# Optimization experiments

Measured on AMD Instinct MI355X. Metric: run time of the kernel, lower is better.

The kernel has to match this reference:

```python
import jax, jax.numpy as jnp
import numpy as np

PRE_NMS_TOPK = 6000
POST_NMS_TOPK = 1000
NMS_THRESH = 0.7
MIN_SIZE = 16.0
NEG = -1e9  # stand-in for -inf that is safe under autodiff


def setup_inputs() -> dict:
    key = jax.random.key(0)
    k1, k2, k3, k4, k5, k6, k7, k8 = jax.random.split(key, 8)
    B, A = 8, 200000
    N = B * A
    # realistic anchors: centers within a ~1333x800 canvas, sizes 16..256
    cx = jax.random.uniform(k1, (N,), minval=0.0, maxval=1200.0)
    cy = jax.random.uniform(k2, (N,), minval=0.0, maxval=800.0)
    w = jax.random.uniform(k3, (N,), minval=16.0, maxval=256.0)
    h = jax.random.uniform(k4, (N,), minval=16.0, maxval=256.0)
    anchors = jnp.stack([cx - 0.5 * w, cy - 0.5 * h, cx + 0.5 * w, cy + 0.5 * h], axis=1)
    batch_indices = jnp.sort(jax.random.randint(k5, (N,), 0, B)).astype(jnp.int32)
    image_sizes = jax.random.randint(k6, (B, 2), 600, 1334).astype(jnp.int32)  # (H, W)
    objectness_logits = jax.random.normal(k7, (N, 1), dtype=jnp.float32)
    bbox_deltas = jax.random.normal(k8, (N, 4), dtype=jnp.float32) * 0.2
    return {
        'anchors': anchors,
        'batch_indices': batch_indices,
        'image_sizes': image_sizes,
        'objectness_logits': objectness_logits,
        'bbox_deltas': bbox_deltas,
    }


def _nms_one(bx, sc):
    """Greedy NMS on [K,4] boxes / [K] scores; returns POST_NMS_TOPK (idx, ok)."""
    K = bx.shape[0]
    areas = (bx[:, 2] - bx[:, 0]) * (bx[:, 3] - bx[:, 1])
    ar = jnp.arange(K)

    def step(sup, _):
        s = jnp.where(sup, NEG, sc)
        j = jnp.argmax(s)
        ok = s[j] > 0.5 * NEG
        b = bx[j]
        ix1 = jnp.maximum(b[0], bx[:, 0])
        iy1 = jnp.maximum(b[1], bx[:, 1])
        ix2 = jnp.minimum(b[2], bx[:, 2])
        iy2 = jnp.minimum(b[3], bx[:, 3])
        inter = jnp.maximum(ix2 - ix1, 0.0) * jnp.maximum(iy2 - iy1, 0.0)
        iou = inter / (areas + areas[j] - inter + 1e-9)
        sup = sup | (iou > NMS_THRESH) | (ar == j)
        return sup, (j, ok)

    sup0 = sc <= 0.5 * NEG  # padded / invalid entries start suppressed
    _, (idx, ok) = jax.lax.scan(step, sup0, None, length=POST_NMS_TOPK)
    return idx, ok


def reference(anchors, batch_indices, image_sizes, objectness_logits, bbox_deltas):
    B = image_sizes.shape[0]
    N = anchors.shape[0]
    sizes = image_sizes[batch_indices].astype(jnp.float32)  # [N,2] (H,W) per anchor

    # --- box decode ---
    a_w = anchors[:, 2] - anchors[:, 0]
    a_h = anchors[:, 3] - anchors[:, 1]
    a_x = anchors[:, 0] + 0.5 * a_w
    a_y = anchors[:, 1] + 0.5 * a_h
    t_x, t_y = bbox_deltas[:, 0], bbox_deltas[:, 1]
    t_w, t_h = bbox_deltas[:, 2], bbox_deltas[:, 3]
    p_x = a_x + t_x * a_w
    p_y = a_y + t_y * a_h
    p_w = a_w * jnp.exp(jnp.clip(t_w, -10.0, 10.0))
    p_h = a_h * jnp.exp(jnp.clip(t_h, -10.0, 10.0))
    x1 = p_x - 0.5 * p_w
    y1 = p_y - 0.5 * p_h
    x2 = p_x + 0.5 * p_w
    y2 = p_y + 0.5 * p_h

    # --- clip to image ---
    H, W = sizes[:, 0], sizes[:, 1]
    x1 = jnp.clip(x1, 0.0, W - 1.0)
    y1 = jnp.clip(y1, 0.0, H - 1.0)
    x2 = jnp.clip(x2, 0.0, W - 1.0)
    y2 = jnp.clip(y2, 0.0, H - 1.0)
    boxes = jnp.stack([x1, y1, x2, y2], axis=1)  # [N,4]

    # --- min-size filter (as score masking) ---
    valid = ((x2 - x1) >= MIN_SIZE) & ((y2 - y1) >= MIN_SIZE)
    fg = jax.nn.sigmoid(objectness_logits[:, 0])

    # --- per-image top-k over masked scores ---
    img_mask = batch_indices[None, :] == jnp.arange(B, dtype=batch_indices.dtype)[:, None]  # [B,N]
    scores = jnp.where(img_mask & valid[None, :], fg[None, :], NEG)  # [B,N]
    top_scores, top_idx = jax.lax.top_k(scores, PRE_NMS_TOPK)  # [B,PRE]
    top_boxes = boxes[top_idx]  # [B,PRE,4]

    # --- NMS per image ---
    keep_idx, keep_ok = jax.vmap(_nms_one)(top_boxes, top_scores)  # [B,POST]

    sel = jnp.take_along_axis(top_idx, keep_idx, axis=1)  # global anchor indices [B,POST]
    okf = keep_ok[..., None].astype(boxes.dtype)
    props = jnp.take_along_axis(top_boxes, keep_idx[..., None], axis=1) * okf  # [B,POST,4]
    obj = objectness_logits[sel] * okf  # [B,POST,1]
    deltas_out = bbox_deltas[sel] * okf  # [B,POST,4]
    bidx = jnp.where(keep_ok, jnp.arange(B, dtype=jnp.int32)[:, None], -1)  # [B,POST]

    return (props.reshape(-1, 4), bidx.reshape(-1), obj.reshape(-1, 1),
            deltas_out.reshape(-1, 4), keep_ok.reshape(-1))
```

## Files before the change

### kernel.cpp

```cpp
#include <hip/hip_runtime.h>
#include <stdint.h>

#define PRE_K   6000
#define POST_K  1000
#define CAP     8192
#define BINS    1024
#define ROWS    6016
#define CH      94
#define RC_CH   32
#define JSPLIT  8
#define NEGF    -1000000000.0f
#define IOU_EPS 16.0f


__device__ __forceinline__ uint32_t orderf(float f) {
  uint32_t u = __float_as_uint(f);
  return (u & 0x80000000u) ? ~u : (u | 0x80000000u);
}

__device__ __forceinline__ int score_bin(float sc) {
  int bin = (int)floorf((sc + 12.0f) * ((float)BINS / 24.0f));
  return bin < 0 ? 0 : (bin > BINS - 1 ? BINS - 1 : bin);
}

__device__ __forceinline__ int bin_slot(int bin) {
  return ((bin & 15) << 6) | (bin >> 4);
}

__device__ __forceinline__ void decode_box(
    const float* __restrict__ anchors, const float* __restrict__ deltas,
    const int* __restrict__ isz, int n, int b,
    double& x1, double& y1, double& x2, double& y2, bool& valid) {
  double ax1 = (double)anchors[4 * n + 0], ay1 = (double)anchors[4 * n + 1];
  double ax2 = (double)anchors[4 * n + 2], ay2 = (double)anchors[4 * n + 3];
  double aw = ax2 - ax1, ah = ay2 - ay1;
  double acx = ax1 + 0.5 * aw, acy = ay1 + 0.5 * ah;
  double tx = (double)deltas[4 * n + 0], ty = (double)deltas[4 * n + 1];
  double tw = (double)deltas[4 * n + 2], th = (double)deltas[4 * n + 3];
  tw = tw < -10.0 ? -10.0 : (tw > 10.0 ? 10.0 : tw);
  th = th < -10.0 ? -10.0 : (th > 10.0 ? 10.0 : th);
  double px = acx + tx * aw, py = acy + ty * ah;
  double pw = aw * exp(tw), ph = ah * exp(th);
  double H = (double)isz[2 * b + 0], W = (double)isz[2 * b + 1];
  double wm = W - 1.0, hm = H - 1.0;
  x1 = px - 0.5 * pw; y1 = py - 0.5 * ph;
  x2 = px + 0.5 * pw; y2 = py + 0.5 * ph;
  x1 = fmin(fmax(x1, 0.0), wm); x2 = fmin(fmax(x2, 0.0), wm);
  y1 = fmin(fmax(y1, 0.0), hm); y2 = fmin(fmax(y2, 0.0), hm);
  valid = (x2 - x1 >= 16.0) && (y2 - y1 >= 16.0);
}

__device__ __forceinline__ bool iou_exact(const double* __restrict__ tbox,
                                          const double* __restrict__ tarea,
                                          size_t ri, size_t ci) {
  const double* pr = &tbox[ri * 4];
  const double* pc = &tbox[ci * 4];
  double w = fmin(pr[2], pc[2]) - fmax(pr[0], pc[0]); w = w > 0.0 ? w : 0.0;
  double h = fmin(pr[3], pc[3]) - fmax(pr[1], pc[1]); h = h > 0.0 ? h : 0.0;
  double it = w * h;
  return it > 0.7 * (tarea[ri] + tarea[ci] - it + 1e-9);
}


__global__ void __launch_bounds__(256) k_score(const float* __restrict__ anchors,
                                               const int* __restrict__ bix,
                                               const int* __restrict__ isz,
                                               const float* __restrict__ logits,
                                               const float* __restrict__ deltas,
                                               float* __restrict__ scores,
                                               uint32_t* __restrict__ hist, int N) {
  const int SPAN = 4096;
  int start = blockIdx.x * SPAN;
  int end = start + SPAN < N ? start + SPAN : N;
  __shared__ uint32_t lh[2][BINS];
  for (int i = threadIdx.x; i < 2 * BINS; i += 256) ((uint32_t*)lh)[i] = 0u;
  __shared__ int s_b0, s_b1;
  if (threadIdx.x == 0) { s_b0 = bix[start]; s_b1 = bix[end - 1]; }
  __syncthreads();
  int b0 = s_b0, b1 = s_b1;

  for (int n = start + (int)threadIdx.x; n < end; n += 256) {
    int b = bix[n];
    double x1, y1, x2, y2; bool valid;
    decode_box(anchors, deltas, isz, n, b, x1, y1, x2, y2, valid);
    float sc = valid ? logits[n] : NEGF;
    scores[n] = sc;
    if (valid) {
      int bin = score_bin(sc);
      if (b == b0)      atomicAdd(&lh[0][bin], 1u);
      else if (b == b1) atomicAdd(&lh[1][bin], 1u);
      else              atomicAdd(&hist[b * BINS + bin_slot(bin)], 1u);
    }
  }
  __syncthreads();
  for (int bin = threadIdx.x; bin < BINS; bin += 256) {
    uint32_t c0 = lh[0][bin];
    if (c0) atomicAdd(&hist[b0 * BINS + bin_slot(bin)], c0);
    if (b1 != b0) {
      uint32_t c1 = lh[1][bin];
      if (c1) atomicAdd(&hist[b1 * BINS + bin_slot(bin)], c1);
    }
  }
}

__global__ void __launch_bounds__(1024) k_compact(const float* __restrict__ scores,
                                                  const int* __restrict__ bix,
                                                  const uint32_t* __restrict__ hist,
                                                  uint32_t* __restrict__ cnt,
                                                  uint64_t* __restrict__ cand, int N) {
  const int SPAN = 8192;
  int start = blockIdx.x * SPAN;
  int end = start + SPAN < N ? start + SPAN : N;
  int t = threadIdx.x;
  __shared__ int s_b0, s_b1;
  __shared__ uint32_t sh[BINS];
  __shared__ int s_bs;
  __shared__ uint32_t lcnt[8], lbase[8];
  if (t == 0) { s_b0 = bix[start]; s_b1 = bix[end - 1]; }
  if (t < 8) lcnt[t] = 0u;
  __syncthreads();
  int b0 = s_b0, b1 = s_b1;

  uint32_t bs0 = 0, bs1 = 0;
  for (int pass = 0; pass < 2; pass++) {
    int b = pass == 0 ? b0 : b1;
    if (pass == 1 && b1 == b0) { bs1 = bs0; break; }
    if (t < BINS) sh[t] = hist[b * BINS + bin_slot(t)];
    if (t == 0) s_bs = 0;
    __syncthreads();
    for (int off = 1; off < BINS; off <<= 1) {
      uint32_t v = (t < BINS && t + off < BINS) ? sh[t + off] : 0u;
      __syncthreads();
      if (t < BINS) sh[t] += v;
      __syncthreads();
    }
    if (t < BINS && sh[t] >= PRE_K) atomicMax(&s_bs, t);
    __syncthreads();
    if (pass == 0) bs0 = (uint32_t)s_bs; else bs1 = (uint32_t)s_bs;
    __syncthreads();
  }

  bool     predv[8];
  uint64_t keyv[8];
  uint32_t lposv[8];
  int      bv[8];
  int nt = 0;
  for (int base = start; base < end; base += 1024, nt++) {
    int n = base + t;
    bool pred = false; int b = 0; uint64_t key = 0ull; uint32_t lp = 0u;
    if (n < end) {
      float sc = scores[n];
      if (sc > 0.5f * NEGF) {
        b = bix[n];
        uint32_t bs = (b == b0) ? bs0 : bs1;
        if ((uint32_t)score_bin(sc) >= bs) {
          pred = true;
          key = ((uint64_t)orderf(sc) << 32) | (uint64_t)(uint32_t)(~(uint32_t)n);
          lp = atomicAdd(&lcnt[b], 1u);
        }
      }
    }
    predv[nt] = pred; keyv[nt] = key; lposv[nt] = lp; bv[nt] = b;
  }
  __syncthreads();
  if (t < 8) {
    uint32_t c = lcnt[t];
    lbase[t] = c ? atomicAdd(&cnt[t], c) : 0u;
  }
  __syncthreads();
  for (int k = 0; k < nt; k++) {
    if (predv[k]) {
      uint32_t pos = lbase[bv[k]] + lposv[k];
      if (pos < CAP) cand[(size_t)bv[k] * CAP + pos] = keyv[k];
    }
  }
}

__global__ void __launch_bounds__(256) k_rank(const uint64_t* __restrict__ cand,
                                              const uint32_t* __restrict__ cnt,
                                              uint32_t* __restrict__ prank) {
  int blk = blockIdx.x;
  int js = blk % JSPLIT;
  int ic = (blk / JSPLIT) % 32;
  int b  = blk / (JSPLIT * 32);
  int t = threadIdx.x;
  int C = (int)min(cnt[b], (uint32_t)CAP);
  if (ic * 256 >= C) return;
  const uint64_t* g = cand + (size_t)b * CAP;
  int i = ic * 256 + t;
  uint64_t ki = (i < C) ? g[i] : 0ull;

  int q = (C + JSPLIT - 1) / JSPLIT;
  int j0 = js * q;
  int j1 = j0 + q < C ? j0 + q : C;

  __shared__ uint64_t tile[1024];
  int rank = 0;
  for (int base = j0; base < j1; base += 1024) {
#pragma unroll
    for (int u = 0; u < 4; u++) {
      int j = base + u * 256 + t;
      tile[u * 256 + t] = (j < j1) ? g[j] : 0ull;
    }
    __syncthreads();
    int lim = j1 - base < 1024 ? j1 - base : 1024;
    const ulonglong2* t2 = (const ulonglong2*)tile;
    int pairs = lim >> 1;
    int jj = 0;
    for (; jj + 4 <= pairs; jj += 4) {
      ulonglong2 v0 = t2[jj + 0], v1 = t2[jj + 1];
      ulonglong2 v2 = t2[jj + 2], v3 = t2[jj + 3];
      rank += (v0.x > ki) ? 1 : 0; rank += (v0.y > ki) ? 1 : 0;
      rank += (v1.x > ki) ? 1 : 0; rank += (v1.y > ki) ? 1 : 0;
      rank += (v2.x > ki) ? 1 : 0; rank += (v2.y > ki) ? 1 : 0;
      rank += (v3.x > ki) ? 1 : 0; rank += (v3.y > ki) ? 1 : 0;
    }
    for (; jj < pairs; jj++) {
      ulonglong2 v = t2[jj];
      rank += (v.x > ki) ? 1 : 0; rank += (v.y > ki) ? 1 : 0;
    }
    if (lim & 1) rank += (tile[lim - 1] > ki) ? 1 : 0;
    __syncthreads();
  }
  if (i < C) prank[((size_t)b * JSPLIT + js) * CAP + i] = (uint32_t)rank;
}

__global__ void __launch_bounds__(256) k_place_gather(
    const uint64_t* __restrict__ cand, const uint32_t* __restrict__ cnt,
    const uint32_t* __restrict__ prank,
    const float* __restrict__ anchors, const float* __restrict__ deltas,
    const int* __restrict__ isz,
    double* __restrict__ tbox, double* __restrict__ tarea,
    float4* __restrict__ tboxf, float* __restrict__ tareaf,
    int* __restrict__ top_n, int* __restrict__ Cnum, int B) {
  int idx = blockIdx.x * blockDim.x + threadIdx.x;
  if (idx >= B * CAP) return;
  int b = idx / CAP, i = idx % CAP;
  int C = (int)min(cnt[b], (uint32_t)CAP);
  if (i == 0) Cnum[b] = C < PRE_K ? C : PRE_K;
  if (i >= C) return;
  uint32_t rank = 0;
#pragma unroll
  for (int js = 0; js < JSPLIT; js++)
    rank += prank[((size_t)b * JSPLIT + js) * CAP + i];
  if (rank >= PRE_K) return;
  int n = (int)(~(uint32_t)(cand[idx] & 0xFFFFFFFFull));
  double x1, y1, x2, y2; bool valid;
  decode_box(anchors, deltas, isz, n, b, x1, y1, x2, y2, valid);
  size_t row = (size_t)b * ROWS + rank;
  tbox[row * 4 + 0] = x1;
  tbox[row * 4 + 1] = y1;
  tbox[row * 4 + 2] = x2;
  tbox[row * 4 + 3] = y2;
  double ar = (x2 - x1) * (y2 - y1);
  tarea[row] = ar;
  tboxf[row] = make_float4((float)x1, (float)y1, (float)x2, (float)y2);
  tareaf[row] = (float)ar;
  top_n[b * PRE_K + rank] = n;
}

__global__ void __launch_bounds__(64) k_iou_mat(const float4* __restrict__ tboxf,
                                                const float* __restrict__ tareaf,
                                                const double* __restrict__ tbox,
                                                const double* __restrict__ tarea,
                                                const int* __restrict__ Cnum,
                                                uint32_t* __restrict__ maskT) {
  int blk = blockIdx.x;
  int k  = blk % (RC_CH + 1);
  int cc = (blk / (RC_CH + 1)) % CH;
  int b  = blk / ((RC_CH + 1) * CH);
  int rc = (k == RC_CH) ? cc : k;
  if (k < RC_CH && cc <= rc) return;
  int C = Cnum[b];
  if (rc * 64 >= C || cc * 64 >= C) return;
  int lane = threadIdx.x;
  size_t bb = (size_t)b * ROWS;

  float4 cb4 = tboxf[bb + (size_t)cc * 64 + lane];
  float  sca = 0.7f * tareaf[bb + (size_t)cc * 64 + lane];
  __shared__ float4 rbx[64];
  __shared__ float  rsa[64];
  rbx[lane] = tboxf[bb + (size_t)rc * 64 + lane];
  rsa[lane] = 0.7f * tareaf[bb + (size_t)rc * 64 + lane];
  __syncthreads();

  bool isdiag = (rc == cc);
  uint32_t res0 = 0u, res1 = 0u;

  for (int i = 0; i < 64; i++) {
    float4 r4 = rbx[i];
    float sra = rsa[i];
    float iw = fminf(r4.z, cb4.z) - fmaxf(r4.x, cb4.x);
    float ih = fminf(r4.w, cb4.w) - fmaxf(r4.y, cb4.y);
    iw = fmaxf(iw, 0.0f); ih = fmaxf(ih, 0.0f);
    float inter = iw * ih;
    float diff = fmaf(1.7f, inter, -(sra + sca));
    bool gt = isdiag ? (lane > i) : true;
    unsigned long long sup   = __ballot(gt && (diff >  IOU_EPS));
    unsigned long long loose = __ballot(gt && (diff > -IOU_EPS));
    unsigned long long border = loose & ~sup;
    if (border) {
      bool mine = (border >> lane) & 1ull;
      bool ex = false;
      if (mine)
        ex = iou_exact(tbox, tarea, bb + (size_t)rc * 64 + i,
                       bb + (size_t)cc * 64 + lane);
      sup |= __ballot(ex);
    }
    if (lane == i) { res0 = (uint32_t)sup; res1 = (uint32_t)(sup >> 32); }
  }
  uint2* seg = (uint2*)(maskT + (((size_t)b * CH + cc) * ROWS + (size_t)rc * 64) * 2);
  seg[lane] = make_uint2(res0, res1);
}

__global__ void __launch_bounds__(256) k_nms_reduce(const uint32_t* __restrict__ maskT,
                                                    const float4* __restrict__ tboxf,
                                                    const float* __restrict__ tareaf,
                                                    const double* __restrict__ tbox,
                                                    const double* __restrict__ tarea,
                                                    const int* __restrict__ Cnum,
                                                    const int* __restrict__ top_n,
                                                    const float* __restrict__ logits,
                                                    const float* __restrict__ deltas,
                                                    float* __restrict__ out, int B) {
  int b = blockIdx.x, t = threadIdx.x;
  int wave = t >> 6, lane = t & 63;
  int C = Cnum[b];
  const uint32_t* M = maskT + (size_t)b * CH * ROWS * 2;
  size_t bb = (size_t)b * ROWS;

  __shared__ uint32_t s_f[2][2];
  __shared__ uint32_t kept_lo[POST_K];
  __shared__ uint32_t kept_hi[POST_K];
  __shared__ uint64_t s_kept;
  if (t < 4) ((uint32_t*)s_f)[t] = 0u;

  uint32_t d0 = 0u, d1 = 0u;
  if (wave == 0) {
    const uint32_t* rp = M + (size_t)lane * 2;
    d0 = rp[0]; d1 = rp[1];
  }
  __syncthreads();

  int nkept = 0, nlo = 0, nhi = 0;
  for (int c = 0; c < CH; c++) {
    int base = c * 64;
    if (base >= C) break;
    int cbuf = c & 1;
    if (t == 0) { s_f[cbuf ^ 1][0] = 0u; s_f[cbuf ^ 1][1] = 0u; }

    uint32_t f0 = 0u, f1 = 0u;
    for (int k2 = t; k2 < nlo; k2 += 256) {
      const uint32_t* rp = M + ((size_t)c * ROWS + kept_lo[k2]) * 2;
      f0 |= rp[0]; f1 |= rp[1];
    }
    if (nhi > 0) {
      float4 cb4 = tboxf[bb + base + lane];
      float  sca = 0.7f * tareaf[bb + base + lane];
      for (int k2 = wave; k2 < nhi; k2 += 4) {
        int r = (int)kept_hi[k2];
        float4 r4 = tboxf[bb + r];
        float sra = 0.7f * tareaf[bb + r];
        float iw = fminf(r4.z, cb4.z) - fmaxf(r4.x, cb4.x);
        float ih = fminf(r4.w, cb4.w) - fmaxf(r4.y, cb4.y);
        iw = fmaxf(iw, 0.0f); ih = fmaxf(ih, 0.0f);
        float inter = iw * ih;
        float diff = fmaf(1.7f, inter, -(sra + sca));
        unsigned long long sup   = __ballot(diff >  IOU_EPS);
        unsigned long long loose = __ballot(diff > -IOU_EPS);
        unsigned long long border = loose & ~sup;
        if (border) {
          bool mine = (border >> lane) & 1ull;
          bool ex = false;
          if (mine) ex = iou_exact(tbox, tarea, bb + r, bb + base + lane);
          sup |= __ballot(ex);
        }
        f0 |= (uint32_t)sup; f1 |= (uint32_t)(sup >> 32);
      }
    }
#pragma unroll
    for (int off = 32; off > 0; off >>= 1) {
      f0 |= (uint32_t)__shfl_xor((int)f0, off, 64);
      f1 |= (uint32_t)__shfl_xor((int)f1, off, 64);
    }
    if (lane == 0 && (f0 | f1)) {
      atomicOr(&s_f[cbuf][0], f0);
      atomicOr(&s_f[cbuf][1], f1);
    }
    __syncthreads();

    if (wave == 0) {
      uint64_t sup = (uint64_t)s_f[cbuf][0] | ((uint64_t)s_f[cbuf][1] << 32);
      int rem = C - base;
      if (rem < 64) sup |= ~((1ull << rem) - 1ull);
      uint64_t diag = (uint64_t)d0 | ((uint64_t)d1 << 32);
      int cn = (c + 1 < CH) ? c + 1 : c;
      const uint32_t* rpn = M + ((size_t)cn * ROWS + (size_t)cn * 64 + lane) * 2;
      uint32_t pn0 = rpn[0], pn1 = rpn[1];

      uint64_t keptMask = 0ull;
      uint64_t alive = ~sup;
      uint64_t m = alive;
      while (m) {
        int i = __builtin_ctzll(m);
        keptMask |= 1ull << i;
        uint64_t d = (uint64_t)__shfl((long long)diag, i, 64);
        sup |= d | (1ull << i);
        m = alive & ~sup;
      }
      int allowed = POST_K - nkept;
      int pc = __popcll(keptMask);
      while (pc > allowed) {
        keptMask &= ~(1ull << (63 - __builtin_clzll(keptMask)));
        pc--;
      }
      if (lane == 0) s_kept = keptMask;
      if ((keptMask >> lane) & 1ull) {
        int pfx = __popcll(keptMask & ((1ull << lane) - 1ull));
        int row = base + lane;
        if (c < RC_CH) kept_lo[nlo + pfx] = (uint32_t)row;
        else           kept_hi[nhi + pfx] = (uint32_t)row;
      }
      d0 = pn0; d1 = pn1;
    }
    __syncthreads();

    int pc = __popcll(s_kept);
    nkept += pc;
    if (c < RC_CH) nlo += pc; else nhi += pc;
    if (nkept >= POST_K) break;
  }

  __syncthreads();
  int M_out = B * POST_K;
  for (int s2 = t; s2 < POST_K; s2 += 256) {
    float p0 = 0.f, p1 = 0.f, p2 = 0.f, p3 = 0.f;
    float ob = 0.f, d0f = 0.f, d1f = 0.f, d2f = 0.f, d3f = 0.f;
    float bi = -1.0f, okv = 0.0f;
    if (s2 < nkept) {
      int j = (s2 < nlo) ? (int)kept_lo[s2] : (int)kept_hi[s2 - nlo];
      int n = top_n[b * PRE_K + j];
      const double* p = &tbox[(bb + j) * 4];
      p0 = (float)p[0]; p1 = (float)p[1]; p2 = (float)p[2]; p3 = (float)p[3];
      ob = logits[n];
      d0f = deltas[4 * n + 0]; d1f = deltas[4 * n + 1];
      d2f = deltas[4 * n + 2]; d3f = deltas[4 * n + 3];
      bi = (float)b; okv = 1.0f;
    }
    int idx = b * POST_K + s2;
    out[idx * 4 + 0] = p0;
    out[idx * 4 + 1] = p1;
    out[idx * 4 + 2] = p2;
    out[idx * 4 + 3] = p3;
    out[4 * M_out + idx] = bi;
    out[5 * M_out + idx] = ob;
    out[6 * M_out + idx * 4 + 0] = d0f;
    out[6 * M_out + idx * 4 + 1] = d1f;
    out[6 * M_out + idx * 4 + 2] = d2f;
    out[6 * M_out + idx * 4 + 3] = d3f;
    out[10 * M_out + idx] = okv;
  }
}


extern "C" void kernel_launch(void* const* d_in, const int* in_sizes, int n_in,
                              void* d_out, int out_size, void* d_ws, size_t ws_size,
                              hipStream_t stream) {
  const float* anchors = (const float*)d_in[0];
  const int*   bix     = (const int*)d_in[1];
  const int*   isz     = (const int*)d_in[2];
  const float* logits  = (const float*)d_in[3];
  const float* deltas  = (const float*)d_in[4];
  float* out = (float*)d_out;

  int N = in_sizes[1];
  int B = in_sizes[2] / 2;

  uintptr_t p = (uintptr_t)d_ws;
  double*   tbox   = (double*)p;    p += (size_t)B * ROWS * 4 * sizeof(double);
  double*   tarea  = (double*)p;    p += (size_t)B * ROWS * sizeof(double);
  uint64_t* cand   = (uint64_t*)p;  p += (size_t)B * CAP * sizeof(uint64_t);
  float*    scores = (float*)p;     p += (size_t)N * sizeof(float);
  uint32_t* hist   = (uint32_t*)p;  p += (size_t)B * BINS * sizeof(uint32_t);
  uint32_t* cnt    = (uint32_t*)p;  p += (size_t)B * sizeof(uint32_t);
  uint32_t* prank  = (uint32_t*)p;  p += (size_t)B * JSPLIT * CAP * sizeof(uint32_t);
  int*      top_n    = (int*)p;     p += (size_t)B * PRE_K * sizeof(int);
  int*      Cnum     = (int*)p;      p += (size_t)B * sizeof(int);
  p = (p + 255) & ~(uintptr_t)255;
  uint32_t* maskT    = (uint32_t*)p; p += (size_t)B * CH * ROWS * 2 * sizeof(uint32_t);
  float4*   tboxf  = (float4*)scores;
  float*    tareaf = (float*)(scores + (size_t)B * ROWS * 4);
  (void)ws_size; (void)n_in; (void)out_size;

  hipMemsetAsync(hist, 0, (size_t)(B * BINS + B) * sizeof(uint32_t), stream);
  k_score<<<(N + 4095) / 4096, 256, 0, stream>>>(anchors, bix, isz, logits, deltas,
                                                 scores, hist, N);
  k_compact<<<(N + 8191) / 8192, 1024, 0, stream>>>(scores, bix, hist, cnt, cand, N);
  k_rank<<<B * 32 * JSPLIT, 256, 0, stream>>>(cand, cnt, prank);
  k_place_gather<<<(B * CAP + 255) / 256, 256, 0, stream>>>(cand, cnt, prank,
                                                            anchors, deltas, isz,
                                                            tbox, tarea, tboxf,
                                                            tareaf, top_n, Cnum, B);
  k_iou_mat<<<B * CH * (RC_CH + 1), 64, 0, stream>>>(tboxf, tareaf, tbox, tarea,
                                                     Cnum, maskT);
  k_nms_reduce<<<B, 256, 0, stream>>>(maskT, tboxf, tareaf, tbox, tarea, Cnum,
                                      top_n, logits, deltas, out, B);
}
```

Before: 353.5 us.

## Compute full upper-triangular IoU mask and push suppression forward during NMS scan

The IoU mask kernel now fills every upper-triangular 64x64 tile over a 3D grid, replacing the hybrid where only the first 32 row chunks were precomputed and later chunks recomputed IoU on the fly. The NMS reduce kernel changes from pulling kept rows per chunk to pushing them forward. Rows kept in chunk c are OR-ed into per-chunk shared accumulators for all later chunks by waves 1-3, while wave 0 resolves chunk c+1 using the next-chunk rows it prefetched. This removes the on-the-fly IoU recomputation and overlaps mask accumulation with the serial greedy scan. In exchange it computes a much larger mask (about 94*95/2 tiles per image), which costs more memory traffic and more shared-memory atomics.

```diff
diff --git a/kernel.cpp b/kernel.cpp
--- a/kernel.cpp
+++ b/kernel.cpp
@@ -7,7 +7,6 @@
 #define BINS    1024
 #define ROWS    6016
 #define CH      94
-#define RC_CH   32
 #define JSPLIT  8
 #define NEGF    -1000000000.0f
 #define IOU_EPS 16.0f
@@ -265,14 +264,12 @@
                                                 const double* __restrict__ tarea,
                                                 const int* __restrict__ Cnum,
                                                 uint32_t* __restrict__ maskT) {
-  int blk = blockIdx.x;
-  int k  = blk % (RC_CH + 1);
-  int cc = (blk / (RC_CH + 1)) % CH;
-  int b  = blk / ((RC_CH + 1) * CH);
-  int rc = (k == RC_CH) ? cc : k;
-  if (k < RC_CH && cc <= rc) return;
+  int rc = blockIdx.x;
+  int cc = blockIdx.y;
+  int b  = blockIdx.z;
+  if (rc > cc) return;
   int C = Cnum[b];
-  if (rc * 64 >= C || cc * 64 >= C) return;
+  if (cc * 64 >= C) return;
   int lane = threadIdx.x;
   size_t bb = (size_t)b * ROWS;
 
@@ -314,10 +311,7 @@
 }
 
 __global__ void __launch_bounds__(256) k_nms_reduce(const uint32_t* __restrict__ maskT,
-                                                    const float4* __restrict__ tboxf,
-                                                    const float* __restrict__ tareaf,
                                                     const double* __restrict__ tbox,
-                                                    const double* __restrict__ tarea,
                                                     const int* __restrict__ Cnum,
                                                     const int* __restrict__ top_n,
                                                     const float* __restrict__ logits,
@@ -326,78 +320,40 @@
   int b = blockIdx.x, t = threadIdx.x;
   int wave = t >> 6, lane = t & 63;
   int C = Cnum[b];
-  const uint32_t* M = maskT + (size_t)b * CH * ROWS * 2;
+  int nch = (C + 63) >> 6;
+  const uint32_t* Mb = maskT + (size_t)b * CH * ROWS * 2;
   size_t bb = (size_t)b * ROWS;
 
-  __shared__ uint32_t s_f[2][2];
-  __shared__ uint32_t kept_lo[POST_K];
-  __shared__ uint32_t kept_hi[POST_K];
+  __shared__ uint32_t acc[CH][2];
+  __shared__ uint16_t kept[POST_K];
+  __shared__ uint16_t pend[2][64];
+  __shared__ int      npend[2];
   __shared__ uint64_t s_kept;
-  if (t < 4) ((uint32_t*)s_f)[t] = 0u;
-
-  uint32_t d0 = 0u, d1 = 0u;
-  if (wave == 0) {
-    const uint32_t* rp = M + (size_t)lane * 2;
-    d0 = rp[0]; d1 = rp[1];
-  }
-  __syncthreads();
-
-  int nkept = 0, nlo = 0, nhi = 0;
-  for (int c = 0; c < CH; c++) {
-    int base = c * 64;
-    if (base >= C) break;
-    int cbuf = c & 1;
-    if (t == 0) { s_f[cbuf ^ 1][0] = 0u; s_f[cbuf ^ 1][1] = 0u; }
-
-    uint32_t f0 = 0u, f1 = 0u;
-    for (int k2 = t; k2 < nlo; k2 += 256) {
-      const uint32_t* rp = M + ((size_t)c * ROWS + kept_lo[k2]) * 2;
-      f0 |= rp[0]; f1 |= rp[1];
-    }
-    if (nhi > 0) {
-      float4 cb4 = tboxf[bb + base + lane];
-      float  sca = 0.7f * tareaf[bb + base + lane];
-      for (int k2 = wave; k2 < nhi; k2 += 4) {
-        int r = (int)kept_hi[k2];
-        float4 r4 = tboxf[bb + r];
-        float sra = 0.7f * tareaf[bb + r];
-        float iw = fminf(r4.z, cb4.z) - fmaxf(r4.x, cb4.x);
-        float ih = fminf(r4.w, cb4.w) - fmaxf(r4.y, cb4.y);
-        iw = fmaxf(iw, 0.0f); ih = fmaxf(ih, 0.0f);
-        float inter = iw * ih;
-        float diff = fmaf(1.7f, inter, -(sra + sca));
-        unsigned long long sup   = __ballot(diff >  IOU_EPS);
-        unsigned long long loose = __ballot(diff > -IOU_EPS);
-        unsigned long long border = loose & ~sup;
-        if (border) {
-          bool mine = (border >> lane) & 1ull;
-          bool ex = false;
-          if (mine) ex = iou_exact(tbox, tarea, bb + r, bb + base + lane);
-          sup |= __ballot(ex);
-        }
-        f0 |= (uint32_t)sup; f1 |= (uint32_t)(sup >> 32);
-      }
-    }
-#pragma unroll
-    for (int off = 32; off > 0; off >>= 1) {
-      f0 |= (uint32_t)__shfl_xor((int)f0, off, 64);
-      f1 |= (uint32_t)__shfl_xor((int)f1, off, 64);
-    }
-    if (lane == 0 && (f0 | f1)) {
-      atomicOr(&s_f[cbuf][0], f0);
-      atomicOr(&s_f[cbuf][1], f1);
-    }
-    __syncthreads();
+
+  for (int i = t; i < CH * 2; i += 256) ((uint32_t*)acc)[i] = 0u;
+  if (t < 2) npend[t] = 0;
+  __syncthreads();
+
+  uint2 dgv = make_uint2(0u, 0u), pfv = make_uint2(0u, 0u);
+  if (wave == 0 && nch > 0) {
+    const uint2* pd = (const uint2*)(Mb + ((size_t)0 * ROWS + lane) * 2);
+    dgv = pd[0];
+    if (nch > 1) {
+      const uint2* pp = (const uint2*)(Mb + ((size_t)1 * ROWS + lane) * 2);
+      pfv = pp[0];
+    }
+  }
+
+  int nkept = 0;
+  for (int c = 0; c < nch; c++) {
+    int par = c & 1;
+    int base = c << 6;
 
     if (wave == 0) {
-      uint64_t sup = (uint64_t)s_f[cbuf][0] | ((uint64_t)s_f[cbuf][1] << 32);
+      uint64_t sup = (uint64_t)acc[c][0] | ((uint64_t)acc[c][1] << 32);
       int rem = C - base;
       if (rem < 64) sup |= ~((1ull << rem) - 1ull);
-      uint64_t diag = (uint64_t)d0 | ((uint64_t)d1 << 32);
-      int cn = (c + 1 < CH) ? c + 1 : c;
-      const uint32_t* rpn = M + ((size_t)cn * ROWS + (size_t)cn * 64 + lane) * 2;
-      uint32_t pn0 = rpn[0], pn1 = rpn[1];
-
+      uint64_t diag = (uint64_t)dgv.x | ((uint64_t)dgv.y << 32);
       uint64_t keptMask = 0ull;
       uint64_t alive = ~sup;
       uint64_t m = alive;
@@ -409,25 +365,57 @@
         m = alive & ~sup;
       }
       int allowed = POST_K - nkept;
-      int pc = __popcll(keptMask);
-      while (pc > allowed) {
+      int pc2 = __popcll(keptMask);
+      while (pc2 > allowed) {
         keptMask &= ~(1ull << (63 - __builtin_clzll(keptMask)));
-        pc--;
-      }
-      if (lane == 0) s_kept = keptMask;
+        pc2--;
+      }
+      if (lane == 0) { s_kept = keptMask; npend[par ^ 1] = pc2; }
       if ((keptMask >> lane) & 1ull) {
         int pfx = __popcll(keptMask & ((1ull << lane) - 1ull));
-        int row = base + lane;
-        if (c < RC_CH) kept_lo[nlo + pfx] = (uint32_t)row;
-        else           kept_hi[nhi + pfx] = (uint32_t)row;
-      }
-      d0 = pn0; d1 = pn1;
+        kept[nkept + pfx] = (uint16_t)(base + lane);
+        pend[par ^ 1][pfx] = (uint16_t)(base + lane);
+      }
+      if (c + 1 < nch) {
+        uint32_t v0 = ((keptMask >> lane) & 1ull) ? pfv.x : 0u;
+        uint32_t v1 = ((keptMask >> lane) & 1ull) ? pfv.y : 0u;
+#pragma unroll
+        for (int off = 32; off > 0; off >>= 1) {
+          v0 |= (uint32_t)__shfl_xor((int)v0, off, 64);
+          v1 |= (uint32_t)__shfl_xor((int)v1, off, 64);
+        }
+        if (lane == 0) {
+          if (v0) atomicOr(&acc[c + 1][0], v0);
+          if (v1) atomicOr(&acc[c + 1][1], v1);
+        }
+        const uint2* pd = (const uint2*)(Mb + (((size_t)(c + 1)) * ROWS + base + 64 + lane) * 2);
+        dgv = pd[0];
+        if (c + 2 < nch) {
+          const uint2* pp = (const uint2*)(Mb + (((size_t)(c + 2)) * ROWS + base + 64 + lane) * 2);
+          pfv = pp[0];
+        }
+      }
+    } else {
+      int np = npend[par];
+      int cc0 = c + 1;
+      int span = nch - cc0;
+      if (np > 0 && span > 0) {
+        int total = np * span;
+        for (int it = t - 64; it < total; it += 192) {
+          int pi = it / span;
+          int cc = cc0 + (it - pi * span);
+          int row = (int)pend[par][pi];
+          const uint2* pm = (const uint2*)(Mb + ((size_t)cc * ROWS + row) * 2);
+          uint2 mv = pm[0];
+          if (mv.x) atomicOr(&acc[cc][0], mv.x);
+          if (mv.y) atomicOr(&acc[cc][1], mv.y);
+        }
+      }
     }
     __syncthreads();
 
     int pc = __popcll(s_kept);
     nkept += pc;
-    if (c < RC_CH) nlo += pc; else nhi += pc;
     if (nkept >= POST_K) break;
   }
 
@@ -438,7 +426,7 @@
     float ob = 0.f, d0f = 0.f, d1f = 0.f, d2f = 0.f, d3f = 0.f;
     float bi = -1.0f, okv = 0.0f;
     if (s2 < nkept) {
-      int j = (s2 < nlo) ? (int)kept_lo[s2] : (int)kept_hi[s2 - nlo];
+      int j = (int)kept[s2];
       int n = top_n[b * PRE_K + j];
       const double* p = &tbox[(bb + j) * 4];
       p0 = (float)p[0]; p1 = (float)p[1]; p2 = (float)p[2]; p3 = (float)p[3];
@@ -501,8 +489,8 @@
                                                             anchors, deltas, isz,
                                                             tbox, tarea, tboxf,
                                                             tareaf, top_n, Cnum, B);
-  k_iou_mat<<<B * CH * (RC_CH + 1), 64, 0, stream>>>(tboxf, tareaf, tbox, tarea,
-                                                     Cnum, maskT);
-  k_nms_reduce<<<B, 256, 0, stream>>>(maskT, tboxf, tareaf, tbox, tarea, Cnum,
-                                      top_n, logits, deltas, out, B);
-}
+  dim3 iou_grid(CH, CH, B);
+  k_iou_mat<<<iou_grid, 64, 0, stream>>>(tboxf, tareaf, tbox, tarea, Cnum, maskT);
+  k_nms_reduce<<<B, 256, 0, stream>>>(maskT, tbox, Cnum, top_n, logits, deltas,
+                                      out, B);
+}
```

Result: slower. 419.2 us (+18.6%).
